# Optimization experiments

Measured on AMD Instinct MI355X. Metric: run time of the kernel, lower is better.

The kernel has to match this reference:

```python
import jax, jax.numpy as jnp
import numpy as np

B, S, D, H, L, V, DFF = 8, 1024, 256, 8, 4, 100, 1024
EPS = 1e-5


def _pos_encodings(seq_len, d):
    # Faithful to SinusoidalPositionalEmbedding (NOTE: original uses sin for both halves)
    pos = jnp.arange(seq_len, dtype=jnp.float32)[:, None]        # [S,1]
    freqs = jnp.arange(d, dtype=jnp.float32)[None, :]            # [1,D]
    sin_even = jnp.sin(pos / 10000.0 ** (freqs[:, 0::2] / d))    # [S,D/2]
    sin_odd = jnp.sin(pos / 10000.0 ** (freqs[:, 1::2] / d))     # [S,D/2]
    return jnp.concatenate([sin_even, sin_odd], axis=1)          # [S,D]


def _self_attention_mask(sequence_length, seq_len):
    # create_self_attention_mask with causal=True; assumes max(sequence_length)==seq_len
    r = jnp.arange(seq_len)[None, :]                             # [1,S]
    m = (r < sequence_length[:, None]).astype(jnp.float32)       # [B,S]
    m = m[:, :, None] * m[:, None, :]                            # [B,S,S]
    causal = jnp.tril(jnp.ones((seq_len, seq_len), jnp.float32))
    return m * causal                                            # [B,S,S]


def setup_inputs() -> dict:
    key = jax.random.key(0)
    ks = jax.random.split(key, 20)
    n = lambda k, shape, s=0.02: (jax.random.normal(k, shape) * s).astype(jnp.float32)
    return {
        "output_ids": jax.random.randint(ks[0], (B, S), 0, V),
        "target_sequence_length": jnp.full((B,), S, dtype=jnp.int32),
        "embedding": n(ks[1], (V, D), 1.0),
        "Wq": n(ks[2], (L, D, D)), "bq": jnp.zeros((L, D), jnp.float32),
        "Wk": n(ks[3], (L, D, D)), "bk": jnp.zeros((L, D), jnp.float32),
        "Wv": n(ks[4], (L, D, D)), "bv": jnp.zeros((L, D), jnp.float32),
        "Wo": n(ks[5], (L, D, D)), "bo": jnp.zeros((L, D), jnp.float32),
        "W1": n(ks[6], (L, D, DFF)), "b1": jnp.zeros((L, DFF), jnp.float32),
        "W2": n(ks[7], (L, DFF, D)), "b2": jnp.zeros((L, D), jnp.float32),
        "g1": jnp.ones((L, D), jnp.float32), "be1": jnp.zeros((L, D), jnp.float32),
        "g2": jnp.ones((L, D), jnp.float32), "be2": jnp.zeros((L, D), jnp.float32),
        "Wc": n(ks[8], (D, V)), "bc": jnp.zeros((V,), jnp.float32),
    }


def _forward(output_ids, target_sequence_length, embedding, Wq, bq, Wk, bk, Wv, bv,
             Wo, bo, W1, b1, W2, b2, g1, be1, g2, be2, Wc, bc):
    Bn, Sn = output_ids.shape
    d = embedding.shape[1]
    x = embedding[output_ids] + _pos_encodings(Sn, d)[None]      # [B,S,D]
    mask = _self_attention_mask(target_sequence_length, Sn)[:, None] > 0  # [B,1,S,S] bool

    def ln(h, g, b):
        m = h.mean(-1, keepdims=True)
        v = jnp.var(h, axis=-1, keepdims=True)
        return (h - m) / jnp.sqrt(v + EPS) * g + b

    def step(x, p):
        wq, bq_, wk, bk_, wv, bv_, wo, bo_, w1, b1_, w2, b2_, g1_, be1_, g2_, be2_ = p
        q = (x @ wq + bq_).reshape(Bn, Sn, H, -1)
        k = (x @ wk + bk_).reshape(Bn, Sn, H, -1)
        v = (x @ wv + bv_).reshape(Bn, Sn, H, -1)
        dh = q.shape[-1]
        scores = jnp.einsum('bqhd,bkhd->bhqk', q, k) / jnp.sqrt(jnp.float32(dh))
        attn = jax.nn.softmax(jnp.where(mask, scores, -1e9), axis=-1)
        attn = jnp.where(mask, attn, 0.0)                        # post-softmax mask (as original)
        y = jnp.einsum('bhqk,bkhd->bqhd', attn, v).reshape(Bn, Sn, -1)
        y = y @ wo + bo_
        x = ln(x + y, g1_, be1_)
        ff = jax.nn.relu(x @ w1 + b1_) @ w2 + b2_
        x = ln(x + ff, g2_, be2_)
        return x, None

    x, _ = jax.lax.scan(step, x, (Wq, bq, Wk, bk, Wv, bv, Wo, bo, W1, b1, W2, b2, g1, be1, g2, be2))
    return x @ Wc + bc                                           # logits [B,S,V]


def reference(output_ids, target_sequence_length, embedding, Wq, bq, Wk, bk, Wv, bv,
              Wo, bo, W1, b1, W2, b2, g1, be1, g2, be2, Wc, bc):
    return _forward(output_ids, target_sequence_length, embedding, Wq, bq, Wk, bk, Wv, bv,
                    Wo, bo, W1, b1, W2, b2, g1, be1, g2, be2, Wc, bc)
```

## Files before the change

kernel.cpp:

```cpp
#include <hip/hip_runtime.h>
#include <hip/hip_bf16.h>
#include <stdint.h>

#define B_   8
#define S_   1024
#define D_   256
#define H_   8
#define DH_  32
#define L_   4
#define V_   100
#define DFF_ 1024
#define M_   (B_*S_)

using bf16 = __hip_bfloat16;
typedef __bf16 bf16x8 __attribute__((ext_vector_type(8)));
typedef float  f32x4  __attribute__((ext_vector_type(4)));

static __device__ __forceinline__ float b2f(unsigned short u) {
  union { unsigned int i; float f; } w; w.i = ((unsigned int)u) << 16; return w.f;
}
static __device__ __forceinline__ unsigned short f2b(float f) {
  bf16 h = (bf16)f; return *(unsigned short*)&h;
}

static __device__ __forceinline__ void load_lds16(const void* g, void* l) {
  __builtin_amdgcn_global_load_lds((const __attribute__((address_space(1))) void*)g,
                                   (__attribute__((address_space(3))) void*)l,
                                   16, 0, 0);
}

#define SRC_CHS(tid)  ((((tid) & 3) ^ (((tid) >> 3) & 3)) * 8)
#define FRAG_Q8(quad, l15)  (((quad) ^ (((l15) >> 1) & 3)) * 8)

#define GCH64(tid)  ((((tid) & 7) ^ (((tid) >> 3) & 7)) * 8)
#define FQ64(kh, quad, l15)  (((((kh)*4 + (quad)) ^ ((l15) & 7))) * 8)

template<int CTRL>
static __device__ __forceinline__ float dppf(float v) {
  union { float f; int i; } a, r;
  a.f = v;
  r.i = __builtin_amdgcn_update_dpp(0, a.i, CTRL, 0xF, 0xF, true);
  return r.f;
}
static __device__ __forceinline__ float red_sum16(float v) {
  v += dppf<0xB1>(v);
  v += dppf<0x4E>(v);
  v += dppf<0x141>(v);
  v += dppf<0x140>(v);
  return v;
}

__global__ void prep_t(const float* __restrict__ Wq, const float* __restrict__ Wk,
                       const float* __restrict__ Wv, const float* __restrict__ Wo,
                       const float* __restrict__ W1, const float* __restrict__ W2,
                       const float* __restrict__ Wc,
                       const float* __restrict__ bq, const float* __restrict__ bk,
                       const float* __restrict__ bv,
                       const int* __restrict__ ids, const float* __restrict__ emb,
                       bf16* __restrict__ WqkvT, bf16* __restrict__ WoT,
                       bf16* __restrict__ W1T, bf16* __restrict__ W2T,
                       bf16* __restrict__ WcT, float* __restrict__ bqkv,
                       bf16* __restrict__ x)
{
  const int z = blockIdx.z;
  const int tid = threadIdx.y*32 + threadIdx.x;
  if (z >= 26) {
    const int bs = (z - 26)*1024 + blockIdx.y*32 + blockIdx.x;
    const int d  = tid;
    const int s  = bs & (S_-1);
    const int id = ids[bs];
    const int f  = (d < 128) ? (2*d) : (2*(d-128)+1);
    const float inv = powf(10000.f, -(float)f * (1.f/256.f));
    const float pe  = sinf((float)s * inv);
    x[(size_t)bs*D_ + d] = (bf16)(emb[(size_t)id*D_ + d] + pe);
    return;
  }
  if (z == 25) {
    if (blockIdx.x || blockIdx.y) return;
    for (int i = tid; i < L_*768; i += 256) {
      const int l2 = i / 768, j = i % 768;
      const float* src = (j < 256) ? bq : (j < 512) ? bk : bv;
      bqkv[i] = src[l2*256 + (j & 255)];
    }
    return;
  }
  const float* src; bf16* dst; int R, C, Cd;
  if (z < 12) {
    const int l = z / 3, w = z % 3;
    src = ((w == 0) ? Wq : (w == 1) ? Wk : Wv) + (size_t)l*65536;
    R = 256; C = 256; Cd = 256;
    dst = WqkvT + (size_t)l*196608 + (size_t)w*65536;
  } else if (z < 16) {
    const int l = z - 12;
    src = Wo + (size_t)l*65536; R = 256; C = 256; Cd = 256;
    dst = WoT + (size_t)l*65536;
  } else if (z < 20) {
    const int l = z - 16;
    src = W1 + (size_t)l*262144; R = 256; C = 1024; Cd = 1024;
    dst = W1T + (size_t)l*262144;
  } else if (z < 24) {
    const int l = z - 20;
    src = W2 + (size_t)l*262144; R = 1024; C = 256; Cd = 256;
    dst = W2T + (size_t)l*262144;
  } else {
    src = Wc; R = 256; C = 100; Cd = 128;
    dst = WcT;
  }
  const int c0 = blockIdx.x*32, r0 = blockIdx.y*32;
  if (c0 >= Cd || r0 >= R) return;
  __shared__ float t[32][33];
  #pragma unroll
  for (int i = 0; i < 4; ++i) {
    const int r = r0 + threadIdx.y + i*8;
    const int c = c0 + threadIdx.x;
    t[threadIdx.y + i*8][threadIdx.x] = (r < R && c < C) ? src[(size_t)r*C + c] : 0.f;
  }
  __syncthreads();
  #pragma unroll
  for (int i = 0; i < 4; ++i) {
    const int c = c0 + threadIdx.y + i*8;
    const int r = r0 + threadIdx.x;
    if (c < Cd && r < R)
      dst[(size_t)c*R + r] = (bf16)t[threadIdx.x][threadIdx.y + i*8];
  }
}

__global__ __launch_bounds__(256) void gemm_qkv(
    const bf16* __restrict__ A, const bf16* __restrict__ BT,
    const float* __restrict__ bias,
    bf16* __restrict__ qp, bf16* __restrict__ kp, bf16* __restrict__ vt)
{
  __shared__ bf16 As[128*64];
  __shared__ bf16 Bs[64*64];
  __shared__ bf16 Vs[64][136];
  const int tid  = threadIdx.x;
  const int lane = tid & 63, wave = tid >> 6;
  const int quad = lane >> 4, l15 = lane & 15;
  const int m0 = blockIdx.x * 128;
  const int n0 = blockIdx.y * 64;
  const int wm = (wave & 1) * 64;
  const int wn = (wave >> 1) * 32;
  const int K = 256;

  const bf16* a0 = A  + (size_t)m0 * K;
  const bf16* b0 = BT + (size_t)n0 * K;
  const int row32 = tid >> 3;
  const int gch   = GCH64(tid);
  const int l7    = l15 & 7;

  f32x4 acc[4][2] = {};

  for (int k0 = 0; k0 < K; k0 += 64) {
    __syncthreads();
    #pragma unroll
    for (int i = 0; i < 4; ++i)
      load_lds16(a0 + (size_t)(32*i + row32)*K + k0 + gch,
                 (char*)As + i*4096 + (size_t)wave*1024);
    #pragma unroll
    for (int i = 0; i < 2; ++i)
      load_lds16(b0 + (size_t)(32*i + row32)*K + k0 + gch,
                 (char*)Bs + i*4096 + (size_t)wave*1024);
    __syncthreads();
    #pragma unroll
    for (int kh = 0; kh < 2; ++kh) {
      const int fq = (((kh*4 + quad) ^ l7)) * 8;
      bf16x8 af[4], bfr[2];
      #pragma unroll
      for (int mt = 0; mt < 4; ++mt)
        af[mt] = *(const bf16x8*)(As + (wm + mt*16 + l15)*64 + fq);
      #pragma unroll
      for (int nt = 0; nt < 2; ++nt)
        bfr[nt] = *(const bf16x8*)(Bs + (wn + nt*16 + l15)*64 + fq);
      #pragma unroll
      for (int mt = 0; mt < 4; ++mt)
        #pragma unroll
        for (int nt = 0; nt < 2; ++nt)
          acc[mt][nt] = __builtin_amdgcn_mfma_f32_16x16x32_bf16(af[mt], bfr[nt], acc[mt][nt], 0, 0, 0);
    }
  }

  const int seg = n0 >> 8;
  const int b  = m0 >> 10;
  const int s0 = m0 & 1023;

  if (seg < 2) {
    bf16* dst = seg ? kp : qp;
    const float sc = seg ? 1.f : (0.17677669529663687f * 1.4426950408889634f);
    #pragma unroll
    for (int nt = 0; nt < 2; ++nt) {
      const int n  = n0 + wn + nt*16 + l15;
      const int nn = n & 255;
      const int h = nn >> 5, d = nn & 31;
      const float bvs = bias[n];
      bf16* hb = dst + (((size_t)b*H_ + h)*S_)*DH_ + d;
      #pragma unroll
      for (int mt = 0; mt < 4; ++mt) {
        const int ml = wm + mt*16 + quad*4;
        #pragma unroll
        for (int r = 0; r < 4; ++r)
          hb[(size_t)(s0 + ml + r)*DH_] = (bf16)((acc[mt][nt][r] + bvs) * sc);
      }
    }
  } else {
    #pragma unroll
    for (int nt = 0; nt < 2; ++nt) {
      const int nl = wn + nt*16 + l15;
      const float bvs = bias[n0 + nl];
      #pragma unroll
      for (int mt = 0; mt < 4; ++mt) {
        const int ml = wm + mt*16 + quad*4;
        #pragma unroll
        for (int r = 0; r < 4; ++r)
          Vs[nl][ml + r] = (bf16)(acc[mt][nt][r] + bvs);
      }
    }
    __syncthreads();
    #pragma unroll
    for (int t = 0; t < 2; ++t) {
      const int vrow = (tid >> 3) + 32*t;
      const int soff = (tid & 7) * 16;
      const int nn = (n0 + vrow) & 255;
      const int h = nn >> 5, d = nn & 31;
      bf16* dst = vt + (((size_t)b*H_ + h)*DH_ + d)*S_ + s0 + soff;
      *(bf16x8*)dst       = *(const bf16x8*)&Vs[vrow][soff];
      *(bf16x8*)(dst + 8) = *(const bf16x8*)&Vs[vrow][soff + 8];
    }
  }
}

template<bool RELU, bool OUT_BF16>
__global__ __launch_bounds__(256) void gemm_bt(
    const bf16* __restrict__ A, const bf16* __restrict__ BT,
    const float* __restrict__ bias, void* __restrict__ C,
    int M, int N, int K)
{
  __shared__ bf16 As[128*64];
  __shared__ bf16 Bs[64*64];
  const int tid  = threadIdx.x;
  const int lane = tid & 63, wave = tid >> 6;
  const int quad = lane >> 4, l15 = lane & 15;
  const int m0 = blockIdx.x * 128;
  const int n0 = blockIdx.y * 64;
  const int wm = (wave & 1) * 64;
  const int wn = (wave >> 1) * 32;

  const bf16* a0 = A  + (size_t)m0 * K;
  const bf16* b0 = BT + (size_t)n0 * K;
  const int row32 = tid >> 3;
  const int gch   = GCH64(tid);
  const int l7    = l15 & 7;

  f32x4 acc[4][2] = {};

  for (int k0 = 0; k0 < K; k0 += 64) {
    __syncthreads();
    #pragma unroll
    for (int i = 0; i < 4; ++i)
      load_lds16(a0 + (size_t)(32*i + row32)*K + k0 + gch,
                 (char*)As + i*4096 + (size_t)wave*1024);
    #pragma unroll
    for (int i = 0; i < 2; ++i)
      load_lds16(b0 + (size_t)(32*i + row32)*K + k0 + gch,
                 (char*)Bs + i*4096 + (size_t)wave*1024);
    __syncthreads();
    #pragma unroll
    for (int kh = 0; kh < 2; ++kh) {
      const int fq = (((kh*4 + quad) ^ l7)) * 8;
      bf16x8 af[4], bfr[2];
      #pragma unroll
      for (int mt = 0; mt < 4; ++mt)
        af[mt] = *(const bf16x8*)(As + (wm + mt*16 + l15)*64 + fq);
      #pragma unroll
      for (int nt = 0; nt < 2; ++nt)
        bfr[nt] = *(const bf16x8*)(Bs + (wn + nt*16 + l15)*64 + fq);
      #pragma unroll
      for (int mt = 0; mt < 4; ++mt)
        #pragma unroll
        for (int nt = 0; nt < 2; ++nt)
          acc[mt][nt] = __builtin_amdgcn_mfma_f32_16x16x32_bf16(af[mt], bfr[nt], acc[mt][nt], 0, 0, 0);
    }
  }

  #pragma unroll
  for (int nt = 0; nt < 2; ++nt) {
    const int n = n0 + wn + nt*16 + l15;
    const float bvs = bias[n];
    #pragma unroll
    for (int mt = 0; mt < 4; ++mt) {
      const int mr = m0 + wm + mt*16 + quad*4;
      #pragma unroll
      for (int r = 0; r < 4; ++r) {
        float v = acc[mt][nt][r] + bvs;
        if (RELU) v = fmaxf(v, 0.f);
        if (OUT_BF16) ((bf16*)C)[(size_t)(mr + r)*N + n] = (bf16)v;
        else          ((float*)C)[(size_t)(mr + r)*N + n] = v;
      }
    }
  }
}

template<bool RELU, bool OUT_BF16, bool NMASK>
__global__ __launch_bounds__(256) void gemm_bt64(
    const bf16* __restrict__ A, const bf16* __restrict__ BT,
    const float* __restrict__ bias, void* __restrict__ C,
    int M, int N, int K)
{
  __shared__ bf16 As[64*32];
  __shared__ bf16 Bs[64*32];
  const int tid  = threadIdx.x;
  const int lane = tid & 63, wave = tid >> 6;
  const int quad = lane >> 4, l15 = lane & 15;
  const int m0 = blockIdx.x * 64;
  const int n0 = blockIdx.y * 64;
  const int wm = (wave & 1) * 32;
  const int wn = (wave >> 1) * 32;

  const bf16* a0 = A  + (size_t)m0 * K;
  const bf16* b0 = BT + (size_t)n0 * K;
  const int row = tid >> 2;
  const int chs = SRC_CHS(tid);
  const int q8  = FRAG_Q8(quad, l15);

  f32x4 acc[2][2] = {};

  for (int k0 = 0; k0 < K; k0 += 32) {
    __syncthreads();
    load_lds16(a0 + (size_t)row*K + k0 + chs, (char*)As + (size_t)wave*1024);
    load_lds16(b0 + (size_t)row*K + k0 + chs, (char*)Bs + (size_t)wave*1024);
    __syncthreads();
    bf16x8 af[2], bfr[2];
    #pragma unroll
    for (int mt = 0; mt < 2; ++mt)
      af[mt] = *(const bf16x8*)(As + (wm + mt*16 + l15)*32 + q8);
    #pragma unroll
    for (int nt = 0; nt < 2; ++nt)
      bfr[nt] = *(const bf16x8*)(Bs + (wn + nt*16 + l15)*32 + q8);
    #pragma unroll
    for (int mt = 0; mt < 2; ++mt)
      #pragma unroll
      for (int nt = 0; nt < 2; ++nt)
        acc[mt][nt] = __builtin_amdgcn_mfma_f32_16x16x32_bf16(af[mt], bfr[nt], acc[mt][nt], 0, 0, 0);
  }

  #pragma unroll
  for (int nt = 0; nt < 2; ++nt) {
    const int n = n0 + wn + nt*16 + l15;
    if (NMASK && n >= N) continue;
    const float bvs = bias[n];
    #pragma unroll
    for (int mt = 0; mt < 2; ++mt) {
      const int mr = m0 + wm + mt*16 + quad*4;
      #pragma unroll
      for (int r = 0; r < 4; ++r) {
        float v = acc[mt][nt][r] + bvs;
        if (RELU) v = fmaxf(v, 0.f);
        if (OUT_BF16) ((bf16*)C)[(size_t)(mr + r)*N + n] = (bf16)v;
        else          ((float*)C)[(size_t)(mr + r)*N + n] = v;
      }
    }
  }
}

__global__ __launch_bounds__(256) void gemm_ln(
    const bf16* __restrict__ A, const bf16* __restrict__ BT,
    const float* __restrict__ bias, const float* __restrict__ g,
    const float* __restrict__ be, bf16* xio, int K)
{
  __shared__ bf16 As[16*64];
  __shared__ bf16 Bs[256*64];
  __shared__ bf16 Xs[16][264];
  __shared__ float sums[4][16][2];

  const int tid  = threadIdx.x;
  const int lane = tid & 63, wave = tid >> 6;
  const int quad = lane >> 4, l15 = lane & 15;
  const int m0 = blockIdx.x * 16;
  const int wn = wave * 64;

  const bf16* a0 = A + (size_t)m0 * K;
  const int row32 = tid >> 3;
  const int gch   = GCH64(tid);
  const int l7    = l15 & 7;

  f32x4 acc[4] = {};

  for (int k0 = 0; k0 < K; k0 += 64) {
    __syncthreads();
    if (wave < 2)
      load_lds16(a0 + (size_t)(wave*8 + (lane >> 3))*K + k0 + GCH64(lane),
                 (char*)As + (size_t)wave*1024);
    #pragma unroll
    for (int j = 0; j < 8; ++j)
      load_lds16(BT + (size_t)(32*j + row32)*K + k0 + gch,
                 (char*)Bs + j*4096 + (size_t)wave*1024);
    __syncthreads();
    #pragma unroll
    for (int kh = 0; kh < 2; ++kh) {
      const int fq = (((kh*4 + quad) ^ l7)) * 8;
      const bf16x8 af = *(const bf16x8*)(As + l15*64 + fq);
      #pragma unroll
      for (int nt = 0; nt < 4; ++nt) {
        const bf16x8 bfr = *(const bf16x8*)(Bs + (wn + nt*16 + l15)*64 + fq);
        acc[nt] = __builtin_amdgcn_mfma_f32_16x16x32_bf16(af, bfr, acc[nt], 0, 0, 0);
      }
    }
  }

  {
    const int xr = tid >> 4, xc = (tid & 15) * 16;
    const bf16* src = xio + (size_t)(m0 + xr)*D_ + xc;
    *(bf16x8*)&Xs[xr][xc]     = *(const bf16x8*)src;
    *(bf16x8*)&Xs[xr][xc + 8] = *(const bf16x8*)(src + 8);
  }
  __syncthreads();

  float v[4][4];
  float bvs[4];
  #pragma unroll
  for (int nt = 0; nt < 4; ++nt) bvs[nt] = bias[wn + nt*16 + l15];
  #pragma unroll
  for (int r = 0; r < 4; ++r) {
    const int rr = quad*4 + r;
    float ls = 0.f, lq = 0.f;
    #pragma unroll
    for (int nt = 0; nt < 4; ++nt) {
      const float y = acc[nt][r] + bvs[nt];
      const float xv = b2f(*(const unsigned short*)&Xs[rr][wn + nt*16 + l15]);
      const float vv = xv + y;
      v[r][nt] = vv;
      ls += vv;
      lq += vv*vv;
    }
    ls = red_sum16(ls);
    lq = red_sum16(lq);
    if (l15 == 0) { sums[wave][rr][0] = ls; sums[wave][rr][1] = lq; }
  }
  __syncthreads();

  float gv[4], bev[4];
  #pragma unroll
  for (int nt = 0; nt < 4; ++nt) {
    gv[nt]  = g[wn + nt*16 + l15];
    bev[nt] = be[wn + nt*16 + l15];
  }
  #pragma unroll
  for (int r = 0; r < 4; ++r) {
    const int rr = quad*4 + r;
    const float ts = sums[0][rr][0] + sums[1][rr][0] + sums[2][rr][0] + sums[3][rr][0];
    const float tq = sums[0][rr][1] + sums[1][rr][1] + sums[2][rr][1] + sums[3][rr][1];
    const float mean = ts * (1.f/256.f);
    const float var  = tq * (1.f/256.f) - mean*mean;
    const float inv  = rsqrtf(var + 1e-5f);
    #pragma unroll
    for (int nt = 0; nt < 4; ++nt) {
      const bf16 o = (bf16)((v[r][nt] - mean)*inv*gv[nt] + bev[nt]);
      Xs[rr][wn + nt*16 + l15] = o;
    }
  }
  __syncthreads();

  {
    const int xr = tid >> 4, xc = (tid & 15) * 16;
    bf16* dst = xio + (size_t)(m0 + xr)*D_ + xc;
    *(bf16x8*)dst       = *(const bf16x8*)&Xs[xr][xc];
    *(bf16x8*)(dst + 8) = *(const bf16x8*)&Xs[xr][xc + 8];
  }
}

#define PSTR 68
__global__ __launch_bounds__(256) void attn_kernel(
    const bf16* __restrict__ qp, const bf16* __restrict__ kp,
    const bf16* __restrict__ vt, const int* __restrict__ tsl,
    bf16* __restrict__ out)
{
  const int h = blockIdx.y, b = blockIdx.z;
  const int lane = threadIdx.x & 63, wave = threadIdx.x >> 6;
  const int quad = lane >> 4, l15 = lane & 15;
  const int sid = blockIdx.x + wave*16;
  const int q0 = sid*16;
  const int len = tsl[b];

  __shared__ bf16 Pl[4][16*PSTR];

  const size_t bh = (size_t)b*H_ + h;
  const bf16* qb = qp + bh*S_*DH_;
  const bf16* kb = kp + bh*S_*DH_;
  const bf16* vb = vt + bh*DH_*S_;

  const bf16x8 qf = *(const bf16x8*)(qb + (size_t)(q0 + l15)*DH_ + quad*8);

  float lacc = 0.f;
  f32x4 o0 = {0.f,0.f,0.f,0.f}, o1 = {0.f,0.f,0.f,0.f};

  bf16* pw = &Pl[wave][0];
  const int qr = q0 + l15;
  const bool full = (len >= S_);
  const int dt = sid >> 2;

  bf16x8 kf[4];
  #pragma unroll
  for (int nt = 0; nt < 4; ++nt)
    kf[nt] = *(const bf16x8*)(kb + (size_t)(nt*16 + l15)*DH_ + quad*8);

  for (int ks = 0; ks <= dt; ++ks) {
    const int k0 = ks*64;
    bf16x8 vf[4];
    #pragma unroll
    for (int kc = 0; kc < 2; ++kc) {
      vf[kc*2]   = *(const bf16x8*)(vb + (size_t)l15*S_      + k0 + kc*32 + quad*8);
      vf[kc*2+1] = *(const bf16x8*)(vb + (size_t)(16+l15)*S_ + k0 + kc*32 + quad*8);
    }
    f32x4 s[4];
    #pragma unroll
    for (int nt = 0; nt < 4; ++nt) {
      const f32x4 z = {0.f,0.f,0.f,0.f};
      s[nt] = __builtin_amdgcn_mfma_f32_16x16x32_bf16(kf[nt], qf, z, 0, 0, 0);
    }
    bf16x8 kn[4];
    if (ks < dt) {
      const int k1 = k0 + 64;
      #pragma unroll
      for (int nt = 0; nt < 4; ++nt)
        kn[nt] = *(const bf16x8*)(kb + (size_t)(k1 + nt*16 + l15)*DH_ + quad*8);
    }
    #pragma unroll
    for (int nt = 0; nt < 4; ++nt) {
      float p0, p1, p2, p3;
      if (full && ks < dt) {
        p0 = exp2f(s[nt][0]);
        p1 = exp2f(s[nt][1]);
        p2 = exp2f(s[nt][2]);
        p3 = exp2f(s[nt][3]);
      } else {
        const int kbase = k0 + nt*16 + quad*4;
        const bool okq = (qr < len);
        p0 = (okq && kbase+0 <= qr && kbase+0 < len) ? exp2f(s[nt][0]) : 0.f;
        p1 = (okq && kbase+1 <= qr && kbase+1 < len) ? exp2f(s[nt][1]) : 0.f;
        p2 = (okq && kbase+2 <= qr && kbase+2 < len) ? exp2f(s[nt][2]) : 0.f;
        p3 = (okq && kbase+3 <= qr && kbase+3 < len) ? exp2f(s[nt][3]) : 0.f;
      }
      lacc += (p0 + p1) + (p2 + p3);
      uint2 w;
      w.x = (unsigned)f2b(p0) | ((unsigned)f2b(p1) << 16);
      w.y = (unsigned)f2b(p2) | ((unsigned)f2b(p3) << 16);
      *(uint2*)((char*)pw + l15*(PSTR*2) + nt*32 + quad*8) = w;
    }
    asm volatile("s_waitcnt lgkmcnt(0)" ::: "memory");
    #pragma unroll
    for (int kc = 0; kc < 2; ++kc) {
      const bf16x8 pf = *(const bf16x8*)(pw + l15*PSTR + kc*32 + quad*8);
      o0 = __builtin_amdgcn_mfma_f32_16x16x32_bf16(pf, vf[kc*2],   o0, 0, 0, 0);
      o1 = __builtin_amdgcn_mfma_f32_16x16x32_bf16(pf, vf[kc*2+1], o1, 0, 0, 0);
    }
    if (ks < dt) {
      #pragma unroll
      for (int nt = 0; nt < 4; ++nt) kf[nt] = kn[nt];
    }
  }

  float lt = lacc;
  lt += __shfl_xor(lt, 16);
  lt += __shfl_xor(lt, 32);

  bf16* ob = out + (size_t)b*S_*D_ + h*DH_;
  #pragma unroll
  for (int r = 0; r < 4; ++r) {
    const float lr = __shfl(lt, (lane & 48) | (quad*4 + r));
    const float inv = 1.f / fmaxf(lr, 1e-30f);
    const size_t rowoff = (size_t)(q0 + quad*4 + r)*D_;
    ob[rowoff + l15]      = (bf16)(o0[r]*inv);
    ob[rowoff + 16 + l15] = (bf16)(o1[r]*inv);
  }
}

extern "C" void kernel_launch(void* const* d_in, const int* in_sizes, int n_in,
                              void* d_out, int out_size, void* d_ws, size_t ws_size,
                              hipStream_t stream)
{
  const int*   ids = (const int*)d_in[0];
  const int*   tsl = (const int*)d_in[1];
  const float* emb = (const float*)d_in[2];
  const float* Wq  = (const float*)d_in[3];
  const float* bq  = (const float*)d_in[4];
  const float* Wk  = (const float*)d_in[5];
  const float* bk  = (const float*)d_in[6];
  const float* Wv  = (const float*)d_in[7];
  const float* bv  = (const float*)d_in[8];
  const float* Wo  = (const float*)d_in[9];
  const float* bo  = (const float*)d_in[10];
  const float* W1  = (const float*)d_in[11];
  const float* b1  = (const float*)d_in[12];
  const float* W2  = (const float*)d_in[13];
  const float* b2  = (const float*)d_in[14];
  const float* g1  = (const float*)d_in[15];
  const float* be1 = (const float*)d_in[16];
  const float* g2  = (const float*)d_in[17];
  const float* be2 = (const float*)d_in[18];
  const float* Wc  = (const float*)d_in[19];
  const float* bc  = (const float*)d_in[20];

  if (ws_size < (size_t)40*1024*1024) return;

  char* p = (char*)d_ws;
  auto carve = [&](size_t bytes) { void* r = (void*)p; p += (bytes + 255) & ~(size_t)255; return r; };
  bf16*  x     = (bf16*) carve((size_t)M_*D_*2);
  char*  big   = (char*) carve((size_t)M_*DFF_*2);
  char*  pkbuf = (char*) carve((size_t)12*1024*1024);
  bf16*  WqkvT = (bf16*) carve((size_t)L_*768*256*2);
  bf16*  WoT   = (bf16*) carve((size_t)L_*65536*2);
  bf16*  W1T   = (bf16*) carve((size_t)L_*262144*2);
  bf16*  W2T   = (bf16*) carve((size_t)L_*262144*2);
  bf16*  WcT   = (bf16*) carve((size_t)128*256*2);
  float* bqkv  = (float*)carve((size_t)L_*768*4);

  bf16*  aout = (bf16*)big;
  bf16*  ff1  = (bf16*)big;
  bf16*  qp   = (bf16*)pkbuf;
  bf16*  kp   = (bf16*)(pkbuf + (size_t)4*1024*1024);
  bf16*  vt   = (bf16*)(pkbuf + (size_t)8*1024*1024);

  prep_t<<<dim3(32,32,34), dim3(32,8), 0, stream>>>(Wq,Wk,Wv,Wo,W1,W2,Wc,bq,bk,bv,
                                                    ids, emb,
                                                    WqkvT,WoT,W1T,W2T,WcT,bqkv, x);

  for (int l = 0; l < L_; ++l) {
    gemm_qkv<<<dim3(64,12), 256, 0, stream>>>(
        x, WqkvT + (size_t)l*768*256, bqkv + l*768, qp, kp, vt);
    attn_kernel<<<dim3(16,8,8), 256, 0, stream>>>(qp, kp, vt, tsl, aout);
    gemm_ln<<<dim3(512), 256, 0, stream>>>(
        aout, WoT + (size_t)l*65536, bo + l*256, g1 + l*256, be1 + l*256, x, 256);
    gemm_bt<true,true><<<dim3(64,16), 256, 0, stream>>>(
        x, W1T + (size_t)l*262144, b1 + l*1024, ff1, M_, 1024, 256);
    gemm_ln<<<dim3(512), 256, 0, stream>>>(
        ff1, W2T + (size_t)l*262144, b2 + l*256, g2 + l*256, be2 + l*256, x, 1024);
  }

  gemm_bt64<false,false,true><<<dim3(128,2), 256, 0, stream>>>(
      x, WcT, bc, (float*)d_out, M_, V_, 256);
}
```

Measured before the change: 425.0 us.

## Software-pipeline attention: compute next P tile while multiplying current P by V

Restructures the causal attention loop into a two-stage software pipeline with double-buffered LDS P tiles. The score MFMA and exp for tile ks+1 are issued before the P·V MFMAs of tile ks, and K is prefetched two tiles ahead with V one tile ahead. This is meant to hide the LDS round-trip wait and global-load latency inside each wave. In exchange it doubles the per-wave LDS for P and raises register pressure. It also drops the explicit lgkmcnt wait and relies on the compiler to order the LDS write and read within the wave.

```diff
diff --git a/kernel.cpp b/kernel.cpp
--- a/kernel.cpp
+++ b/kernel.cpp
@@ -33,7 +33,6 @@
 #define FRAG_Q8(quad, l15)  (((quad) ^ (((l15) >> 1) & 3)) * 8)
 
 #define GCH64(tid)  ((((tid) & 7) ^ (((tid) >> 3) & 7)) * 8)
-#define FQ64(kh, quad, l15)  (((((kh)*4 + (quad)) ^ ((l15) & 7))) * 8)
 
 template<int CTRL>
 static __device__ __forceinline__ float dppf(float v) {
@@ -480,7 +479,7 @@
   const int q0 = sid*16;
   const int len = tsl[b];
 
-  __shared__ bf16 Pl[4][16*PSTR];
+  __shared__ bf16 Pl[4][2][16*PSTR];
 
   const size_t bh = (size_t)b*H_ + h;
   const bf16* qb = qp + bh*S_*DH_;
@@ -492,41 +491,23 @@
   float lacc = 0.f;
   f32x4 o0 = {0.f,0.f,0.f,0.f}, o1 = {0.f,0.f,0.f,0.f};
 
-  bf16* pw = &Pl[wave][0];
   const int qr = q0 + l15;
   const bool full = (len >= S_);
   const int dt = sid >> 2;
 
-  bf16x8 kf[4];
-  #pragma unroll
-  for (int nt = 0; nt < 4; ++nt)
-    kf[nt] = *(const bf16x8*)(kb + (size_t)(nt*16 + l15)*DH_ + quad*8);
-
-  for (int ks = 0; ks <= dt; ++ks) {
-    const int k0 = ks*64;
-    bf16x8 vf[4];
-    #pragma unroll
-    for (int kc = 0; kc < 2; ++kc) {
-      vf[kc*2]   = *(const bf16x8*)(vb + (size_t)l15*S_      + k0 + kc*32 + quad*8);
-      vf[kc*2+1] = *(const bf16x8*)(vb + (size_t)(16+l15)*S_ + k0 + kc*32 + quad*8);
-    }
+  auto make_p = [&](int t, const bf16x8* kfr) {
+    bf16* pw = &Pl[wave][t & 1][0];
     f32x4 s[4];
     #pragma unroll
     for (int nt = 0; nt < 4; ++nt) {
       const f32x4 z = {0.f,0.f,0.f,0.f};
-      s[nt] = __builtin_amdgcn_mfma_f32_16x16x32_bf16(kf[nt], qf, z, 0, 0, 0);
-    }
-    bf16x8 kn[4];
-    if (ks < dt) {
-      const int k1 = k0 + 64;
-      #pragma unroll
-      for (int nt = 0; nt < 4; ++nt)
-        kn[nt] = *(const bf16x8*)(kb + (size_t)(k1 + nt*16 + l15)*DH_ + quad*8);
-    }
+      s[nt] = __builtin_amdgcn_mfma_f32_16x16x32_bf16(kfr[nt], qf, z, 0, 0, 0);
+    }
+    const int k0 = t*64;
     #pragma unroll
     for (int nt = 0; nt < 4; ++nt) {
       float p0, p1, p2, p3;
-      if (full && ks < dt) {
+      if (full && t < dt) {
         p0 = exp2f(s[nt][0]);
         p1 = exp2f(s[nt][1]);
         p2 = exp2f(s[nt][2]);
@@ -545,16 +526,52 @@
       w.y = (unsigned)f2b(p2) | ((unsigned)f2b(p3) << 16);
       *(uint2*)((char*)pw + l15*(PSTR*2) + nt*32 + quad*8) = w;
     }
-    asm volatile("s_waitcnt lgkmcnt(0)" ::: "memory");
-    #pragma unroll
-    for (int kc = 0; kc < 2; ++kc) {
-      const bf16x8 pf = *(const bf16x8*)(pw + l15*PSTR + kc*32 + quad*8);
-      o0 = __builtin_amdgcn_mfma_f32_16x16x32_bf16(pf, vf[kc*2],   o0, 0, 0, 0);
-      o1 = __builtin_amdgcn_mfma_f32_16x16x32_bf16(pf, vf[kc*2+1], o1, 0, 0, 0);
-    }
+  };
+
+  bf16x8 kf[4], vf[4];
+  #pragma unroll
+  for (int nt = 0; nt < 4; ++nt)
+    kf[nt] = *(const bf16x8*)(kb + (size_t)(nt*16 + l15)*DH_ + quad*8);
+  #pragma unroll
+  for (int kc = 0; kc < 2; ++kc) {
+    vf[kc*2]   = *(const bf16x8*)(vb + (size_t)l15*S_      + kc*32 + quad*8);
+    vf[kc*2+1] = *(const bf16x8*)(vb + (size_t)(16+l15)*S_ + kc*32 + quad*8);
+  }
+  make_p(0, kf);
+  if (dt > 0) {
+    #pragma unroll
+    for (int nt = 0; nt < 4; ++nt)
+      kf[nt] = *(const bf16x8*)(kb + (size_t)(64 + nt*16 + l15)*DH_ + quad*8);
+  }
+
+  for (int ks = 0; ks <= dt; ++ks) {
+    const bf16* rb = &Pl[wave][ks & 1][0];
+    bf16x8 pf[2];
+    pf[0] = *(const bf16x8*)(rb + l15*PSTR + quad*8);
+    pf[1] = *(const bf16x8*)(rb + l15*PSTR + 32 + quad*8);
+
     if (ks < dt) {
-      #pragma unroll
-      for (int nt = 0; nt < 4; ++nt) kf[nt] = kn[nt];
+      make_p(ks + 1, kf);
+      if (ks + 1 < dt) {
+        const int k2 = (ks + 2)*64;
+        #pragma unroll
+        for (int nt = 0; nt < 4; ++nt)
+          kf[nt] = *(const bf16x8*)(kb + (size_t)(k2 + nt*16 + l15)*DH_ + quad*8);
+      }
+    }
+
+    o0 = __builtin_amdgcn_mfma_f32_16x16x32_bf16(pf[0], vf[0], o0, 0, 0, 0);
+    o1 = __builtin_amdgcn_mfma_f32_16x16x32_bf16(pf[0], vf[1], o1, 0, 0, 0);
+    o0 = __builtin_amdgcn_mfma_f32_16x16x32_bf16(pf[1], vf[2], o0, 0, 0, 0);
+    o1 = __builtin_amdgcn_mfma_f32_16x16x32_bf16(pf[1], vf[3], o1, 0, 0, 0);
+
+    if (ks < dt) {
+      const int k1 = (ks + 1)*64;
+      #pragma unroll
+      for (int kc = 0; kc < 2; ++kc) {
+        vf[kc*2]   = *(const bf16x8*)(vb + (size_t)l15*S_      + k1 + kc*32 + quad*8);
+        vf[kc*2+1] = *(const bf16x8*)(vb + (size_t)(16+l15)*S_ + k1 + kc*32 + quad*8);
+      }
     }
   }
 
```

New measurement: 423.5 us. About the same (-0.4%).
